# Optimization experiments

Hardware: AMD Instinct MI355X
Metric: run time of the kernel (lower is better)

The kernel has to match this reference:

```python
import jax, jax.numpy as jnp
import numpy as np

D_MODEL = 1024
NUM_HEADS = 16
HEAD_DIM = D_MODEL // NUM_HEADS
BATCH, SEQ = 2, 2048


def setup_inputs() -> dict:
    key = jax.random.key(0)
    ks = jax.random.split(key, 5)
    scale = 1.0 / np.sqrt(D_MODEL)  # ~xavier magnitude
    x = jax.random.normal(ks[0], (BATCH, SEQ, D_MODEL), dtype=jnp.float32)
    Wq = jax.random.normal(ks[1], (D_MODEL, D_MODEL), dtype=jnp.float32) * scale
    Wk = jax.random.normal(ks[2], (D_MODEL, D_MODEL), dtype=jnp.float32) * scale
    Wv = jax.random.normal(ks[3], (D_MODEL, D_MODEL), dtype=jnp.float32) * scale
    Wo = jax.random.normal(ks[4], (D_MODEL, D_MODEL), dtype=jnp.float32) * scale
    z = jnp.zeros((D_MODEL,), dtype=jnp.float32)
    return {"x": x, "Wq": Wq, "bq": z, "Wk": Wk, "bk": z, "Wv": Wv, "bv": z, "Wo": Wo, "bo": z}


def reference(x, Wq, bq, Wk, bk, Wv, bv, Wo, bo):
    B, S, _ = x.shape
    H, Dh = NUM_HEADS, HEAD_DIM
    # torch Linear convention: y = x @ W^T + b
    q = (x @ Wq.T + bq).reshape(B, S, H, Dh)
    k = (x @ Wk.T + bk).reshape(B, S, H, Dh)
    v = (x @ Wv.T + bv).reshape(B, S, H, Dh)
    # scores: [B, H, S, S]
    scores = jnp.einsum('bqhd,bkhd->bhqk', q, k) / np.sqrt(Dh).astype(np.float32)
    attn = jax.nn.softmax(scores, axis=-1)
    out = jnp.einsum('bhqk,bkhd->bqhd', attn, v).reshape(B, S, H * Dh)
    return out @ Wo.T + bo
```

## Files before the change

kernel.cpp:

```cpp
#include <hip/hip_runtime.h>
#include <hip/hip_bf16.h>

typedef __bf16 bf16;
typedef __bf16 bf16x8 __attribute__((ext_vector_type(8)));
typedef __bf16 bf16x4 __attribute__((ext_vector_type(4)));
typedef float f32x4 __attribute__((ext_vector_type(4)));

constexpr int DM = 1024, NH = 16, DH = 64, NB = 2, SQ = 2048;
constexpr int MTOT = NB * SQ;
constexpr float QSCALE = 0.125f * 1.44269504088896f;

__device__ __forceinline__ void gld_lds16(const bf16* g, bf16* l) {
  __builtin_amdgcn_global_load_lds(
      (const __attribute__((address_space(1))) void*)g,
      (__attribute__((address_space(3))) void*)l, 16, 0, 0);
}

__global__ __launch_bounds__(256) void cvt5(
    const float* __restrict__ s0, const float* __restrict__ s1,
    const float* __restrict__ s2, const float* __restrict__ s3,
    const float* __restrict__ s4,
    bf16* __restrict__ d0, bf16* __restrict__ d1, bf16* __restrict__ d2,
    bf16* __restrict__ d3, bf16* __restrict__ d4) {
  const float* src; bf16* dst; int n;
  switch (blockIdx.y) {
    case 0: src = s0; dst = d0; n = DM * DM; break;
    case 1: src = s1; dst = d1; n = DM * DM; break;
    case 2: src = s2; dst = d2; n = DM * DM; break;
    case 3: src = s3; dst = d3; n = DM * DM; break;
    default: src = s4; dst = d4; n = MTOT * DM; break;
  }
  const int idx = (blockIdx.x * 256 + threadIdx.x) * 4;
  if (idx < n) {
    const float4 v = *(const float4*)(src + idx);
    *(bf16x4*)(dst + idx) = (bf16x4){(bf16)v.x, (bf16)v.y, (bf16)v.z, (bf16)v.w};
  }
}

template <int BM, typename OutT>
__device__ __forceinline__ void gemm_tile(
    const bf16* __restrict__ A, const bf16* __restrict__ Bm,
    const float* __restrict__ bias, OutT* __restrict__ C,
    int rowA0, int rowB0, int N, int K, bool bias_row, float cscale,
    bf16* sA, bf16* sB) {
  constexpr int NT = (BM == 128) ? 4 : 2;
  const int tid = threadIdx.x;
  const int wave = tid >> 6, lane = tid & 63;
  const int quad = lane >> 4, l16 = lane & 15;
  const int row0w = (BM == 128) ? (wave >> 1) * 64 : 0;
  const int col0w = (BM == 128) ? (wave & 1) * 64 : wave * 32;

  f32x4 acc[4][NT];
#pragma unroll
  for (int i = 0; i < 4; i++)
#pragma unroll
    for (int j = 0; j < NT; j++) acc[i][j] = (f32x4){0.f, 0.f, 0.f, 0.f};

  const int srow = lane >> 3;
  const int scol = ((lane & 7) ^ srow) * 8;

  for (int kt = 0; kt < K; kt += 64) {
#pragma unroll
    for (int i = 0; i < BM / 32; i++) {
      const int r = i * 32 + wave * 8;
      gld_lds16(A + (size_t)(rowA0 + r + srow) * K + kt + scol, &sA[r * 64]);
    }
#pragma unroll
    for (int i = 0; i < 4; i++) {
      const int r = i * 32 + wave * 8;
      gld_lds16(Bm + (size_t)(rowB0 + r + srow) * K + kt + scol, &sB[r * 64]);
    }
    __syncthreads();
#pragma unroll
    for (int kk = 0; kk < 64; kk += 32) {
      bf16x8 aF[4], bF[NT];
      const int slot = (((kk >> 3) + quad) ^ (l16 & 7)) << 3;
#pragma unroll
      for (int mt = 0; mt < 4; mt++)
        aF[mt] = *(const bf16x8*)&sA[(row0w + mt * 16 + l16) * 64 + slot];
#pragma unroll
      for (int nt = 0; nt < NT; nt++)
        bF[nt] = *(const bf16x8*)&sB[(col0w + nt * 16 + l16) * 64 + slot];
#pragma unroll
      for (int mt = 0; mt < 4; mt++)
#pragma unroll
        for (int nt = 0; nt < NT; nt++)
          acc[mt][nt] = __builtin_amdgcn_mfma_f32_16x16x32_bf16(aF[mt], bF[nt], acc[mt][nt], 0, 0, 0);
    }
    __syncthreads();
  }

#pragma unroll
  for (int mt = 0; mt < 4; mt++) {
#pragma unroll
    for (int nt = 0; nt < NT; nt++) {
#pragma unroll
      for (int r = 0; r < 4; r++) {
        const int row = rowA0 + row0w + mt * 16 + quad * 4 + r;
        const int col = rowB0 + col0w + nt * 16 + l16;
        const float bb = bias_row ? bias[row] : bias[col];
        C[(size_t)row * N + col] = (OutT)((acc[mt][nt][r] + bb) * cscale);
      }
    }
  }
}

__global__ __launch_bounds__(256, 4) void qkv_gemm(
    const bf16* __restrict__ xb, const bf16* __restrict__ Wqb,
    const bf16* __restrict__ Wkb, const bf16* __restrict__ Wvb,
    const float* __restrict__ bq, const float* __restrict__ bk,
    const float* __restrict__ bv,
    bf16* __restrict__ Qw, bf16* __restrict__ Kw, bf16* __restrict__ VTw) {
  __shared__ alignas(16) bf16 sA[128 * 64];
  __shared__ alignas(16) bf16 sB[128 * 64];
  if (blockIdx.z == 0) {
    gemm_tile<128, bf16>(xb, Wqb, bq, Qw, blockIdx.x * 128, blockIdx.y * 128, DM, DM, false, QSCALE, sA, sB);
  } else if (blockIdx.z == 1) {
    gemm_tile<128, bf16>(xb, Wkb, bk, Kw, blockIdx.x * 128, blockIdx.y * 128, DM, DM, false, 1.0f, sA, sB);
  } else {
    const int id = blockIdx.y * 32 + blockIdx.x;
    gemm_tile<128, bf16>(Wvb, xb, bv, VTw, (id >> 5) * 128, (id & 31) * 128, MTOT, DM, true, 1.0f, sA, sB);
  }
}

__global__ __launch_bounds__(256, 4) void out_gemm(
    const bf16* __restrict__ A, const bf16* __restrict__ Bm,
    const float* __restrict__ bias, float* __restrict__ C) {
  __shared__ alignas(16) bf16 sA[64 * 64];
  __shared__ alignas(16) bf16 sB[128 * 64];
  gemm_tile<64, float>(A, Bm, bias, C, blockIdx.x * 64, blockIdx.y * 128, DM, DM, false, 1.0f, sA, sB);
}

__global__ __launch_bounds__(256, 2) void attn(
    const bf16* __restrict__ Q, const bf16* __restrict__ Kq,
    const bf16* __restrict__ VT, bf16* __restrict__ O) {
  __shared__ alignas(16) bf16 sK[2][128 * 64];
  __shared__ alignas(16) bf16 sV[2][64 * 128];
  __shared__ alignas(16) bf16 sP[4][32 * 64];
  const int tid = threadIdx.x, wave = tid >> 6, lane = tid & 63;
  const int quad = lane >> 4, l16 = lane & 15;
  const int hb = blockIdx.x, qt = blockIdx.y;
  const int h = hb & 15, b = hb >> 4;

  const bf16* Qg = Q + (size_t)(b * SQ + qt * 128) * DM + h * DH;
  const bf16* Kg = Kq + (size_t)(b * SQ) * DM + h * DH;
  const bf16* Vg = VT + (size_t)(h * DH) * MTOT + b * SQ;

  const int srow = lane >> 3, scol = ((lane & 7) ^ srow) * 8;
  const int vrow = lane >> 4;

  auto stageKV = [&](int t, int buf) {
#pragma unroll
    for (int i = 0; i < 4; i++) {
      const int r = (wave * 4 + i) * 8;
      gld_lds16(Kg + (size_t)(t * 128 + r + srow) * DM + scol, &sK[buf][r * 64]);
    }
#pragma unroll
    for (int i = 0; i < 4; i++) {
      const int r = (wave * 4 + i) * 4;
      const int vchunk = (lane & 15) ^ ((r + vrow) & 7);
      gld_lds16(Vg + (size_t)(r + vrow) * MTOT + t * 128 + vchunk * 8, &sV[buf][r * 128]);
    }
  };

  bf16x8 qF[2][2];
#pragma unroll
  for (int mt = 0; mt < 2; mt++)
#pragma unroll
    for (int kkh = 0; kkh < 2; kkh++)
      qF[mt][kkh] = *(const bf16x8*)(Qg + (size_t)(wave * 32 + mt * 16 + l16) * DM +
                                     kkh * 32 + quad * 8);

  bf16x8 onesF;
#pragma unroll
  for (int i = 0; i < 8; i++) onesF[i] = (bf16)1.0f;

  f32x4 l_acc[2];
  f32x4 o_acc[2][4];
#pragma unroll
  for (int mt = 0; mt < 2; mt++) {
    l_acc[mt] = (f32x4){0.f, 0.f, 0.f, 0.f};
#pragma unroll
    for (int n2 = 0; n2 < 4; n2++) o_acc[mt][n2] = (f32x4){0.f, 0.f, 0.f, 0.f};
  }

  stageKV(0, 0);
  for (int t = 0; t < 16; ++t) {
    __syncthreads();
    if (t + 1 < 16) stageKV(t + 1, (t + 1) & 1);
    const bf16* cK = sK[t & 1];
    const bf16* cV = sV[t & 1];

    f32x4 sacc[2][8];
#pragma unroll
    for (int mt = 0; mt < 2; mt++)
#pragma unroll
      for (int nt = 0; nt < 8; nt++) sacc[mt][nt] = (f32x4){0.f, 0.f, 0.f, 0.f};
#pragma unroll
    for (int kk = 0; kk < 64; kk += 32) {
      bf16x8 kF[8];
      const int slot = (((kk >> 3) + quad) ^ (l16 & 7)) << 3;
#pragma unroll
      for (int nt = 0; nt < 8; nt++)
        kF[nt] = *(const bf16x8*)&cK[(nt * 16 + l16) * 64 + slot];
#pragma unroll
      for (int mt = 0; mt < 2; mt++)
#pragma unroll
        for (int nt = 0; nt < 8; nt++)
          sacc[mt][nt] = __builtin_amdgcn_mfma_f32_16x16x32_bf16(kF[nt], qF[mt][kk >> 5],
                                                                 sacc[mt][nt], 0, 0, 0);
    }

#pragma unroll
    for (int half = 0; half < 2; half++) {
#pragma unroll
      for (int mt = 0; mt < 2; mt++) {
        const int row = mt * 16 + l16;
#pragma unroll
        for (int nt4 = 0; nt4 < 4; nt4++) {
          const f32x4 s = sacc[mt][half * 4 + nt4];
          bf16x4 pk;
#pragma unroll
          for (int r = 0; r < 4; r++) pk[r] = (bf16)__builtin_amdgcn_exp2f(s[r]);
          const int c = 2 * nt4 + (quad >> 1);
          *(bf16x4*)&sP[wave][row * 64 + ((c ^ (row & 7)) << 3) + (quad & 1) * 4] = pk;
        }
      }
#pragma unroll
      for (int kk = 0; kk < 64; kk += 32) {
        bf16x8 pF[2], vF[4];
#pragma unroll
        for (int mt = 0; mt < 2; mt++) {
          const int row = mt * 16 + l16;
          const int c = (kk >> 3) + quad;
          pF[mt] = *(const bf16x8*)&sP[wave][row * 64 + ((c ^ (row & 7)) << 3)];
        }
#pragma unroll
        for (int n2 = 0; n2 < 4; n2++) {
          const int ch = ((half * 64 + kk) >> 3) + quad;
          vF[n2] = *(const bf16x8*)&cV[(n2 * 16 + l16) * 128 + ((ch ^ (l16 & 7)) << 3)];
        }
#pragma unroll
        for (int mt = 0; mt < 2; mt++) {
#pragma unroll
          for (int n2 = 0; n2 < 4; n2++)
            o_acc[mt][n2] = __builtin_amdgcn_mfma_f32_16x16x32_bf16(pF[mt], vF[n2],
                                                                    o_acc[mt][n2], 0, 0, 0);
          l_acc[mt] = __builtin_amdgcn_mfma_f32_16x16x32_bf16(pF[mt], onesF, l_acc[mt], 0, 0, 0);
        }
      }
    }
  }

#pragma unroll
  for (int mt = 0; mt < 2; mt++) {
#pragma unroll
    for (int r = 0; r < 4; r++) {
      const float inv = 1.0f / l_acc[mt][r];
      const int row = qt * 128 + wave * 32 + mt * 16 + quad * 4 + r;
#pragma unroll
      for (int n2 = 0; n2 < 4; n2++) {
        const int col = n2 * 16 + l16;
        O[(size_t)(b * SQ + row) * DM + h * DH + col] = (bf16)(o_acc[mt][n2][r] * inv);
      }
    }
  }
}

extern "C" void kernel_launch(void* const* d_in, const int* in_sizes, int n_in,
                              void* d_out, int out_size, void* d_ws, size_t ws_size,
                              hipStream_t stream) {
  const float* x  = (const float*)d_in[0];
  const float* Wq = (const float*)d_in[1];
  const float* bq = (const float*)d_in[2];
  const float* Wk = (const float*)d_in[3];
  const float* bk = (const float*)d_in[4];
  const float* Wv = (const float*)d_in[5];
  const float* bv = (const float*)d_in[6];
  const float* Wo = (const float*)d_in[7];
  const float* bo = (const float*)d_in[8];
  float* out = (float*)d_out;

  bf16* ws   = (bf16*)d_ws;
  bf16* xb   = ws;
  bf16* Wqb  = ws + (size_t)MTOT * DM;
  bf16* Wkb  = Wqb + (size_t)DM * DM;
  bf16* Wvb  = Wkb + (size_t)DM * DM;
  bf16* Wob  = Wvb + (size_t)DM * DM;
  bf16* Qw   = Wob + (size_t)DM * DM;
  bf16* Kw   = Qw + (size_t)MTOT * DM;
  bf16* VTw  = Kw + (size_t)MTOT * DM;
  bf16* Cw   = VTw + (size_t)MTOT * DM;

  const dim3 blk(256);
  cvt5<<<dim3(MTOT * DM / 1024, 5), blk, 0, stream>>>(Wq, Wk, Wv, Wo, x,
                                                      Wqb, Wkb, Wvb, Wob, xb);
  qkv_gemm<<<dim3(32, 8, 3), blk, 0, stream>>>(xb, Wqb, Wkb, Wvb, bq, bk, bv, Qw, Kw, VTw);
  attn<<<dim3(NH * NB, SQ / 128), blk, 0, stream>>>(Qw, Kw, VTw, Cw);
  out_gemm<<<dim3(MTOT / 64, DM / 128), blk, 0, stream>>>(Cw, Wob, bo, out);
}
```

Baseline: 178.5 us.

## Fuse QKV projections into one kernel and compute softmax row sums with shuffles

Replaces the three separate QKV GEMM tile launches with one kernel that stages each x tile once and computes Q, K and transposed V accumulators together. This reduces redundant loads of x. In exchange it uses 128KB of LDS and three accumulator sets, forcing one block per CU and a smaller grid. In attention, the MFMA against a ones vector used for the softmax denominator is replaced by scalar accumulation plus cross-lane shuffles and a small LDS exchange.

```diff
diff --git a/kernel.cpp b/kernel.cpp
--- a/kernel.cpp
+++ b/kernel.cpp
@@ -37,12 +37,103 @@
   }
 }
 
+__global__ __launch_bounds__(256, 1) void qkv_fused(
+    const bf16* __restrict__ xb, const bf16* __restrict__ Wqb,
+    const bf16* __restrict__ Wkb, const bf16* __restrict__ Wvb,
+    const float* __restrict__ bq, const float* __restrict__ bk,
+    const float* __restrict__ bv,
+    bf16* __restrict__ Qw, bf16* __restrict__ Kw, bf16* __restrict__ VTw) {
+  __shared__ alignas(16) bf16 sX[2][128 * 64];
+  __shared__ alignas(16) bf16 sQ[2][128 * 64];
+  __shared__ alignas(16) bf16 sK[2][128 * 64];
+  __shared__ alignas(16) bf16 sV[2][128 * 64];
+  const int tid = threadIdx.x;
+  const int wave = tid >> 6, lane = tid & 63;
+  const int wm = wave >> 1, wn = wave & 1;
+  const int quad = lane >> 4, l16 = lane & 15;
+  const int m0 = blockIdx.x * 128, n0 = blockIdx.y * 128;
+
+  const int srow = lane >> 3;
+  const int scol = ((lane & 7) ^ srow) * 8;
+
+  auto stage = [&](int kt, int buf) {
+#pragma unroll
+    for (int i = 0; i < 4; i++) {
+      const int r = i * 32 + wave * 8;
+      gld_lds16(xb + (size_t)(m0 + r + srow) * DM + kt + scol, &sX[buf][r * 64]);
+      gld_lds16(Wqb + (size_t)(n0 + r + srow) * DM + kt + scol, &sQ[buf][r * 64]);
+      gld_lds16(Wkb + (size_t)(n0 + r + srow) * DM + kt + scol, &sK[buf][r * 64]);
+      gld_lds16(Wvb + (size_t)(n0 + r + srow) * DM + kt + scol, &sV[buf][r * 64]);
+    }
+  };
+
+  f32x4 accq[4][4], acck[4][4], accv[4][4];
+#pragma unroll
+  for (int i = 0; i < 4; i++)
+#pragma unroll
+    for (int j = 0; j < 4; j++) {
+      accq[i][j] = (f32x4){0.f, 0.f, 0.f, 0.f};
+      acck[i][j] = (f32x4){0.f, 0.f, 0.f, 0.f};
+      accv[i][j] = (f32x4){0.f, 0.f, 0.f, 0.f};
+    }
+
+  stage(0, 0);
+  for (int it = 0; it < 16; it++) {
+    __syncthreads();
+    if (it + 1 < 16) stage((it + 1) * 64, (it + 1) & 1);
+    const bf16* cX = sX[it & 1];
+    const bf16* cQ = sQ[it & 1];
+    const bf16* cK = sK[it & 1];
+    const bf16* cV = sV[it & 1];
+#pragma unroll
+    for (int kk = 0; kk < 64; kk += 32) {
+      const int slot = (((kk >> 3) + quad) ^ (l16 & 7)) << 3;
+      bf16x8 xF[4], qF[4], kF[4], vF[4];
+#pragma unroll
+      for (int i = 0; i < 4; i++) {
+        xF[i] = *(const bf16x8*)&cX[(wm * 64 + i * 16 + l16) * 64 + slot];
+        qF[i] = *(const bf16x8*)&cQ[(wn * 64 + i * 16 + l16) * 64 + slot];
+        kF[i] = *(const bf16x8*)&cK[(wn * 64 + i * 16 + l16) * 64 + slot];
+        vF[i] = *(const bf16x8*)&cV[(wn * 64 + i * 16 + l16) * 64 + slot];
+      }
+#pragma unroll
+      for (int mt = 0; mt < 4; mt++)
+#pragma unroll
+        for (int nt = 0; nt < 4; nt++) {
+          accq[mt][nt] = __builtin_amdgcn_mfma_f32_16x16x32_bf16(xF[mt], qF[nt], accq[mt][nt], 0, 0, 0);
+          acck[mt][nt] = __builtin_amdgcn_mfma_f32_16x16x32_bf16(xF[mt], kF[nt], acck[mt][nt], 0, 0, 0);
+          accv[mt][nt] = __builtin_amdgcn_mfma_f32_16x16x32_bf16(vF[mt], xF[nt], accv[mt][nt], 0, 0, 0);
+        }
+    }
+  }
+
+#pragma unroll
+  for (int mt = 0; mt < 4; mt++) {
+#pragma unroll
+    for (int nt = 0; nt < 4; nt++) {
+#pragma unroll
+      for (int r = 0; r < 4; r++) {
+        {
+          const int row = m0 + wm * 64 + mt * 16 + quad * 4 + r;
+          const int col = n0 + wn * 64 + nt * 16 + l16;
+          Qw[(size_t)row * DM + col] = (bf16)((accq[mt][nt][r] + bq[col]) * QSCALE);
+          Kw[(size_t)row * DM + col] = (bf16)(acck[mt][nt][r] + bk[col]);
+        }
+        {
+          const int row = n0 + wn * 64 + mt * 16 + quad * 4 + r;
+          const int col = m0 + wm * 64 + nt * 16 + l16;
+          VTw[(size_t)row * MTOT + col] = (bf16)(accv[mt][nt][r] + bv[row]);
+        }
+      }
+    }
+  }
+}
+
 template <int BM, typename OutT>
 __device__ __forceinline__ void gemm_tile(
     const bf16* __restrict__ A, const bf16* __restrict__ Bm,
     const float* __restrict__ bias, OutT* __restrict__ C,
-    int rowA0, int rowB0, int N, int K, bool bias_row, float cscale,
-    bf16* sA, bf16* sB) {
+    int rowA0, int rowB0, int N, int K, bf16* sA, bf16* sB) {
   constexpr int NT = (BM == 128) ? 4 : 2;
   const int tid = threadIdx.x;
   const int wave = tid >> 6, lane = tid & 63;
@@ -98,28 +189,9 @@
       for (int r = 0; r < 4; r++) {
         const int row = rowA0 + row0w + mt * 16 + quad * 4 + r;
         const int col = rowB0 + col0w + nt * 16 + l16;
-        const float bb = bias_row ? bias[row] : bias[col];
-        C[(size_t)row * N + col] = (OutT)((acc[mt][nt][r] + bb) * cscale);
-      }
-    }
-  }
-}
-
-__global__ __launch_bounds__(256, 4) void qkv_gemm(
-    const bf16* __restrict__ xb, const bf16* __restrict__ Wqb,
-    const bf16* __restrict__ Wkb, const bf16* __restrict__ Wvb,
-    const float* __restrict__ bq, const float* __restrict__ bk,
-    const float* __restrict__ bv,
-    bf16* __restrict__ Qw, bf16* __restrict__ Kw, bf16* __restrict__ VTw) {
-  __shared__ alignas(16) bf16 sA[128 * 64];
-  __shared__ alignas(16) bf16 sB[128 * 64];
-  if (blockIdx.z == 0) {
-    gemm_tile<128, bf16>(xb, Wqb, bq, Qw, blockIdx.x * 128, blockIdx.y * 128, DM, DM, false, QSCALE, sA, sB);
-  } else if (blockIdx.z == 1) {
-    gemm_tile<128, bf16>(xb, Wkb, bk, Kw, blockIdx.x * 128, blockIdx.y * 128, DM, DM, false, 1.0f, sA, sB);
-  } else {
-    const int id = blockIdx.y * 32 + blockIdx.x;
-    gemm_tile<128, bf16>(Wvb, xb, bv, VTw, (id >> 5) * 128, (id & 31) * 128, MTOT, DM, true, 1.0f, sA, sB);
+        C[(size_t)row * N + col] = (OutT)(acc[mt][nt][r] + bias[col]);
+      }
+    }
   }
 }
 
@@ -128,7 +200,7 @@
     const float* __restrict__ bias, float* __restrict__ C) {
   __shared__ alignas(16) bf16 sA[64 * 64];
   __shared__ alignas(16) bf16 sB[128 * 64];
-  gemm_tile<64, float>(A, Bm, bias, C, blockIdx.x * 64, blockIdx.y * 128, DM, DM, false, 1.0f, sA, sB);
+  gemm_tile<64, float>(A, Bm, bias, C, blockIdx.x * 64, blockIdx.y * 128, DM, DM, sA, sB);
 }
 
 __global__ __launch_bounds__(256, 2) void attn(
@@ -171,18 +243,12 @@
       qF[mt][kkh] = *(const bf16x8*)(Qg + (size_t)(wave * 32 + mt * 16 + l16) * DM +
                                      kkh * 32 + quad * 8);
 
-  bf16x8 onesF;
-#pragma unroll
-  for (int i = 0; i < 8; i++) onesF[i] = (bf16)1.0f;
-
-  f32x4 l_acc[2];
+  float l_i[2] = {0.f, 0.f};
   f32x4 o_acc[2][4];
 #pragma unroll
-  for (int mt = 0; mt < 2; mt++) {
-    l_acc[mt] = (f32x4){0.f, 0.f, 0.f, 0.f};
+  for (int mt = 0; mt < 2; mt++)
 #pragma unroll
     for (int n2 = 0; n2 < 4; n2++) o_acc[mt][n2] = (f32x4){0.f, 0.f, 0.f, 0.f};
-  }
 
   stageKV(0, 0);
   for (int t = 0; t < 16; ++t) {
@@ -221,7 +287,11 @@
           const f32x4 s = sacc[mt][half * 4 + nt4];
           bf16x4 pk;
 #pragma unroll
-          for (int r = 0; r < 4; r++) pk[r] = (bf16)__builtin_amdgcn_exp2f(s[r]);
+          for (int r = 0; r < 4; r++) {
+            const float p = __builtin_amdgcn_exp2f(s[r]);
+            l_i[mt] += p;
+            pk[r] = (bf16)p;
+          }
           const int c = 2 * nt4 + (quad >> 1);
           *(bf16x4*)&sP[wave][row * 64 + ((c ^ (row & 7)) << 3) + (quad & 1) * 4] = pk;
         }
@@ -241,22 +311,30 @@
           vF[n2] = *(const bf16x8*)&cV[(n2 * 16 + l16) * 128 + ((ch ^ (l16 & 7)) << 3)];
         }
 #pragma unroll
-        for (int mt = 0; mt < 2; mt++) {
+        for (int mt = 0; mt < 2; mt++)
 #pragma unroll
           for (int n2 = 0; n2 < 4; n2++)
             o_acc[mt][n2] = __builtin_amdgcn_mfma_f32_16x16x32_bf16(pF[mt], vF[n2],
                                                                     o_acc[mt][n2], 0, 0, 0);
-          l_acc[mt] = __builtin_amdgcn_mfma_f32_16x16x32_bf16(pF[mt], onesF, l_acc[mt], 0, 0, 0);
-        }
-      }
-    }
-  }
-
+      }
+    }
+  }
+
+  float* lbuf = (float*)&sP[wave][0];
 #pragma unroll
   for (int mt = 0; mt < 2; mt++) {
+    float v = l_i[mt];
+    v += __shfl_xor(v, 16);
+    v += __shfl_xor(v, 32);
+    if (quad == 0) lbuf[mt * 16 + l16] = v;
+  }
+  __builtin_amdgcn_s_waitcnt(0);
+#pragma unroll
+  for (int mt = 0; mt < 2; mt++) {
+    const f32x4 lv = *(const f32x4*)&lbuf[mt * 16 + quad * 4];
 #pragma unroll
     for (int r = 0; r < 4; r++) {
-      const float inv = 1.0f / l_acc[mt][r];
+      const float inv = 1.0f / lv[r];
       const int row = qt * 128 + wave * 32 + mt * 16 + quad * 4 + r;
 #pragma unroll
       for (int n2 = 0; n2 < 4; n2++) {
@@ -295,7 +373,7 @@
   const dim3 blk(256);
   cvt5<<<dim3(MTOT * DM / 1024, 5), blk, 0, stream>>>(Wq, Wk, Wv, Wo, x,
                                                       Wqb, Wkb, Wvb, Wob, xb);
-  qkv_gemm<<<dim3(32, 8, 3), blk, 0, stream>>>(xb, Wqb, Wkb, Wvb, bq, bk, bv, Qw, Kw, VTw);
+  qkv_fused<<<dim3(32, 8), blk, 0, stream>>>(xb, Wqb, Wkb, Wvb, bq, bk, bv, Qw, Kw, VTw);
   attn<<<dim3(NH * NB, SQ / 128), blk, 0, stream>>>(Qw, Kw, VTw, Cw);
   out_gemm<<<dim3(MTOT / 64, DM / 128), blk, 0, stream>>>(Cw, Wob, bo, out);
 }
```

After: 198.4 us. 11.2% more time.
